# Performance work log

Hardware: AMD Instinct MI355X
Metric: run time of the kernel (lower is better)

Reference implementation:

```python
import jax, jax.numpy as jnp
import numpy as np

B, OBS, T, H = 4096, 16, 32, 512  # batch, encoder length, decode seq_len, hidden_size


def _lstm_cell(x, h, c, Wi, Wh, b):
    # PyTorch gate order: i, f, g, o. b = b_ih + b_hh (mathematically identical).
    g = x @ Wi.T + h @ Wh.T + b
    i, f, gg, o = jnp.split(g, 4, axis=-1)
    c = jax.nn.sigmoid(f) * c + jax.nn.sigmoid(i) * jnp.tanh(gg)
    h = jax.nn.sigmoid(o) * jnp.tanh(c)
    return h, c


def _encode(xs, Wi, Wh, b):
    # xs: [B, T, 4]; returns final (h, c), zero initial state as in nn.LSTM.
    def step(carry, x):
        h, c = _lstm_cell(x, carry[0], carry[1], Wi, Wh, b)
        return (h, c), None
    z = jnp.zeros((xs.shape[0], H), xs.dtype)
    (h, c), _ = jax.lax.scan(step, (z, z), jnp.swapaxes(xs, 0, 1))
    return h, c


def setup_inputs() -> dict:
    key = jax.random.key(0)
    ks = jax.random.split(key, 22)
    s = 0.05
    p = lambda k, shape: (jax.random.normal(k, shape, jnp.float32) * s)
    return {
        "speed": jax.random.normal(ks[0], (B, OBS, 4), jnp.float32),
        "pos": jax.random.normal(ks[1], (B, OBS, 4), jnp.float32),
        "enc_s_Wi": p(ks[2], (4 * H, 4)), "enc_s_Wh": p(ks[3], (4 * H, H)), "enc_s_b": p(ks[4], (4 * H,)),
        "enc_p_Wi": p(ks[5], (4 * H, 4)), "enc_p_Wh": p(ks[6], (4 * H, H)), "enc_p_b": p(ks[7], (4 * H,)),
        "dec_s_Wi": p(ks[8], (4 * H, 4)), "dec_s_Wh": p(ks[9], (4 * H, H)), "dec_s_b": p(ks[10], (4 * H,)),
        "dec_i_Wi": p(ks[11], (4 * H, 4)), "dec_i_Wh": p(ks[12], (4 * H, H)), "dec_i_b": p(ks[13], (4 * H,)),
        "W_fs": p(ks[14], (4, H)), "b_fs": p(ks[15], (4,)),
        "W_fc": p(ks[16], (2, H)), "b_fc": p(ks[17], (2,)),
        "W_emb": p(ks[18], (4, 2)), "b_emb": p(ks[19], (4,)),
    }


def reference(speed, pos,
              enc_s_Wi, enc_s_Wh, enc_s_b,
              enc_p_Wi, enc_p_Wh, enc_p_b,
              dec_s_Wi, dec_s_Wh, dec_s_b,
              dec_i_Wi, dec_i_Wh, dec_i_b,
              W_fs, b_fs, W_fc, b_fc, W_emb, b_emb):
    h_se, c_se = _encode(speed, enc_s_Wi, enc_s_Wh, enc_s_b)
    h_pe, c_pe = _encode(pos, enc_p_Wi, enc_p_Wh, enc_p_b)
    h_s, c_s = h_se + h_pe, c_se + c_pe
    h_i, c_i = h_s, c_s
    last_speed = speed[:, -1, :]
    last_pos = pos[:, -1, :]

    def step(carry, _):
        h_s, c_s, h_i, c_i, ls, lp = carry
        h_s, c_s = _lstm_cell(ls, h_s, c_s, dec_s_Wi, dec_s_Wh, dec_s_b)
        h_i, c_i = _lstm_cell(lp, h_i, c_i, dec_i_Wi, dec_i_Wh, dec_i_b)
        sp = jnp.clip(h_s @ W_fs.T + b_fs, -100.0, 100.0)        # Hardtanh(-100, 100)
        it = jax.nn.relu(h_i @ W_fc.T + b_fc)                     # fc_crossing
        ls = jax.lax.stop_gradient(sp)                            # .detach()
        lp = jax.lax.stop_gradient(jax.nn.relu(it @ W_emb.T + b_emb))  # pos_embedding(.).detach()
        return (h_s, c_s, h_i, c_i, ls, lp), (sp, jax.nn.softmax(it, axis=1))

    carry0 = (h_s, c_s, h_i, c_i, last_speed, last_pos)
    _, (speed_seq, cross_seq) = jax.lax.scan(step, carry0, None, length=T)
    speed_outputs = jnp.swapaxes(speed_seq, 0, 1)   # [B, T, 4]
    # Faithful to the source bug: intention_outputs is never accumulated, so the
    # returned crossing_outputs holds ONLY the last step's softmax: [B, 1, 2].
    crossing_outputs = cross_seq[-1][:, None, :]
    return speed_outputs, crossing_outputs
```

## Files before the change

kernel.cpp:

```cpp
#include <hip/hip_runtime.h>
#include <stdint.h>

#define H 512
#define KAUG 528
#define KT_N 33
#define LROW 536
#define NROW 32
#define WMAT_ELEMS (16 * KT_N * 4 * 512)
#define T_DEC 32
#define B_TOT 4096

typedef __attribute__((ext_vector_type(8))) short short8;
typedef __attribute__((ext_vector_type(16))) float floatx16;

__device__ __forceinline__ unsigned short f2bf(float x) {
  union { float f; unsigned int u; } v; v.f = x;
  unsigned int u = v.u;
  return (unsigned short)((u + 0x7FFFu + ((u >> 16) & 1u)) >> 16);
}
__device__ __forceinline__ float bf2f(unsigned short s) {
  union { unsigned int u; float f; } v; v.u = ((unsigned int)s) << 16;
  return v.f;
}
__device__ __forceinline__ float rcpf(float x) { return __builtin_amdgcn_rcpf(x); }
__device__ __forceinline__ float sigm(float x) { return rcpf(1.0f + __expf(-x)); }
__device__ __forceinline__ float tanh_f(float x) {
  return 1.0f - 2.0f * rcpf(1.0f + __expf(2.0f * x));
}

__global__ void prep_weights(
    const float* __restrict__ Wh_s, const float* __restrict__ Wi_s, const float* __restrict__ b_s,
    const float* __restrict__ Wh_p, const float* __restrict__ Wi_p, const float* __restrict__ b_p,
    const float* __restrict__ Wh_d, const float* __restrict__ Wi_d, const float* __restrict__ b_d,
    const float* __restrict__ Wh_i, const float* __restrict__ Wi_i, const float* __restrict__ b_i,
    short* __restrict__ wpack)
{
  int idx = blockIdx.x * 256 + threadIdx.x;
  const int per = 2048 * KAUG;
  if (idx >= 4 * per) return;
  int mat = idx / per;
  int rem = idx - mat * per;
  int n = rem / KAUG;
  int ka = rem - n * KAUG;
  const float* Wh; const float* Wi; const float* bb;
  if (mat == 0)      { Wh = Wh_s; Wi = Wi_s; bb = b_s; }
  else if (mat == 1) { Wh = Wh_p; Wi = Wi_p; bb = b_p; }
  else if (mat == 2) { Wh = Wh_d; Wi = Wi_d; bb = b_d; }
  else               { Wh = Wh_i; Wi = Wi_i; bb = b_i; }
  float v;
  if (ka < 512)      v = Wh[n * 512 + ka];
  else if (ka < 516) v = Wi[n * 4 + (ka - 512)];
  else if (ka == 516) v = bb[n];
  else               v = 0.0f;
  int g = n >> 9, ntL = (n >> 5) & 15, ni = n & 31;
  int kt = ka >> 4, kh = (ka >> 3) & 1, ks = ka & 7;
  int lanep = kh * 32 + ni;
  wpack[(size_t)mat * WMAT_ELEMS +
        (((((size_t)ntL * KT_N + kt) * 4 + g) << 9) + (lanep << 3) + ks)] = (short)f2bf(v);
}

__device__ __forceinline__ void lstm_step_mfma(
    const short* hl, const short* __restrict__ wm,
    int lane, int wv, float c_reg[16], float hnew[16])
{
  int arow = lane & 31, ahalf = lane >> 5;
  const short* aptr = hl + arow * LROW + ahalf * 8;
  const short* bp = wm + (size_t)wv * (KT_N * 4 * 512) + (lane << 3);
  floatx16 ai = (floatx16)0.0f, af = (floatx16)0.0f, ag = (floatx16)0.0f, ao = (floatx16)0.0f;
  #pragma unroll 3
  for (int kt = 0; kt < KT_N; ++kt) {
    short8 a  = *(const short8*)(aptr + kt * 16);
    short8 b0 = *(const short8*)(bp);
    short8 b1 = *(const short8*)(bp + 512);
    short8 b2 = *(const short8*)(bp + 1024);
    short8 b3 = *(const short8*)(bp + 1536);
    bp += 2048;
    ai = __builtin_amdgcn_mfma_f32_32x32x16_bf16(a, b0, ai, 0, 0, 0);
    af = __builtin_amdgcn_mfma_f32_32x32x16_bf16(a, b1, af, 0, 0, 0);
    ag = __builtin_amdgcn_mfma_f32_32x32x16_bf16(a, b2, ag, 0, 0, 0);
    ao = __builtin_amdgcn_mfma_f32_32x32x16_bf16(a, b3, ao, 0, 0, 0);
  }
  #pragma unroll
  for (int r = 0; r < 16; ++r) {
    float si = sigm(ai[r]);
    float sf = sigm(af[r]);
    float tg = tanh_f(ag[r]);
    float so = sigm(ao[r]);
    float cn = sf * c_reg[r] + si * tg;
    c_reg[r] = cn;
    hnew[r] = so * tanh_f(cn);
  }
}

__device__ __forceinline__ void write_h(short* hl, int lane, int wv, const float hnew[16]) {
  int arow = lane & 31, ahalf = lane >> 5;
  int col = (wv << 5) + arow;
  #pragma unroll
  for (int r = 0; r < 16; ++r) {
    int row = (r & 3) + ((r >> 2) << 3) + (ahalf << 2);
    hl[row * LROW + col] = (short)f2bf(hnew[r]);
  }
}

__global__ __launch_bounds__(1024) void lstm_encoder(
    const float* __restrict__ speed, const float* __restrict__ pos,
    const short* __restrict__ wpack,
    short* __restrict__ h_enc, float* __restrict__ c_enc)
{
  __shared__ short hl[NROW * LROW];
  int tid = threadIdx.x;
  int b = blockIdx.x;
  int xcd = b & 7, slot = b >> 3;
  int enc = xcd >> 2;
  int rg = slot * 4 + (xcd & 3);
  int r0 = rg * 32;
  const float* xin = enc ? pos : speed;
  const short* wm = wpack + (size_t)enc * WMAT_ELEMS;

  for (int i = tid; i < NROW * LROW; i += 1024) hl[i] = 0;
  __syncthreads();
  if (tid < 32) hl[tid * LROW + 516] = (short)0x3F80;
  if (tid < 128) {
    int r = tid >> 2, c = tid & 3;
    hl[r * LROW + 512 + c] = (short)f2bf(xin[(r0 + r) * 64 + c]);
  }
  __syncthreads();

  int lane = tid & 63, wv = tid >> 6;
  float c_reg[16];
  #pragma unroll
  for (int r = 0; r < 16; ++r) c_reg[r] = 0.0f;
  float hnew[16];

  for (int t = 0; t < 16; ++t) {
    lstm_step_mfma(hl, wm, lane, wv, c_reg, hnew);
    __syncthreads();
    write_h(hl, lane, wv, hnew);
    if (t < 15 && tid < 128) {
      int r = tid >> 2, c = tid & 3;
      hl[r * LROW + 512 + c] = (short)f2bf(xin[(r0 + r) * 64 + (t + 1) * 4 + c]);
    }
    __syncthreads();
  }

  for (int i = tid; i < 32 * 512; i += 1024) {
    int r = i >> 9, k = i & 511;
    h_enc[((size_t)(enc * B_TOT + r0 + r) << 9) + k] = hl[r * LROW + k];
  }
  int arow = lane & 31, ahalf = lane >> 5;
  int col = (wv << 5) + arow;
  #pragma unroll
  for (int r = 0; r < 16; ++r) {
    int row = (r & 3) + ((r >> 2) << 3) + (ahalf << 2);
    c_enc[((size_t)(enc * B_TOT + r0 + row) << 9) + col] = c_reg[r];
  }
}

__global__ __launch_bounds__(1024) void lstm_decoder(
    const float* __restrict__ speed, const float* __restrict__ pos,
    const short* __restrict__ wpack,
    const short* __restrict__ h_enc, const float* __restrict__ c_enc,
    const float* __restrict__ W_fs, const float* __restrict__ b_fs,
    const float* __restrict__ W_fc, const float* __restrict__ b_fc,
    const float* __restrict__ W_emb, const float* __restrict__ b_emb,
    float* __restrict__ out)
{
  __shared__ short hl[NROW * LROW];
  int tid = threadIdx.x;
  int b = blockIdx.x;
  int xcd = b & 7, slot = b >> 3;
  int chain = xcd >> 2;
  int rg = slot * 4 + (xcd & 3);
  int r0 = rg * 32;
  const short* wm = wpack + (size_t)(2 + chain) * WMAT_ELEMS;

  for (int i = tid; i < NROW * LROW; i += 1024) hl[i] = 0;
  __syncthreads();
  for (int i = tid; i < 32 * 512; i += 1024) {
    int r = i >> 9, k = i & 511;
    float h0 = bf2f((unsigned short)h_enc[((size_t)(r0 + r) << 9) + k])
             + bf2f((unsigned short)h_enc[((size_t)(B_TOT + r0 + r) << 9) + k]);
    hl[r * LROW + k] = (short)f2bf(h0);
  }
  if (tid < 32) hl[tid * LROW + 516] = (short)0x3F80;
  {
    const float* last = chain ? pos : speed;
    if (tid < 128) {
      int r = tid >> 2, c = tid & 3;
      hl[r * LROW + 512 + c] = (short)f2bf(last[(r0 + r) * 64 + 60 + c]);
    }
  }
  int lane = tid & 63, wv = tid >> 6;
  int arow = lane & 31, ahalf = lane >> 5;
  float c_reg[16];
  {
    int col = (wv << 5) + arow;
    #pragma unroll
    for (int r = 0; r < 16; ++r) {
      int row = (r & 3) + ((r >> 2) << 3) + (ahalf << 2);
      size_t gi = ((size_t)(r0 + row) << 9) + col;
      c_reg[r] = c_enc[gi] + c_enc[gi + (((size_t)B_TOT) << 9)];
    }
  }
  __syncthreads();

  float hnew[16];
  for (int t = 0; t < T_DEC; ++t) {
    lstm_step_mfma(hl, wm, lane, wv, c_reg, hnew);
    __syncthreads();
    write_h(hl, lane, wv, hnew);
    __syncthreads();
    for (int r = 0; r < 2; ++r) {
      int row = wv * 2 + r;
      const short8 hvs = *(const short8*)(hl + row * LROW + lane * 8);
      float hv[8];
      #pragma unroll
      for (int j = 0; j < 8; ++j) hv[j] = bf2f((unsigned short)hvs[j]);
      if (chain == 0) {
        float p0 = 0.f, p1 = 0.f, p2 = 0.f, p3 = 0.f;
        #pragma unroll
        for (int j = 0; j < 8; ++j) {
          p0 += hv[j] * W_fs[0 * 512 + lane * 8 + j];
          p1 += hv[j] * W_fs[1 * 512 + lane * 8 + j];
          p2 += hv[j] * W_fs[2 * 512 + lane * 8 + j];
          p3 += hv[j] * W_fs[3 * 512 + lane * 8 + j];
        }
        #pragma unroll
        for (int off = 32; off > 0; off >>= 1) {
          p0 += __shfl_xor(p0, off);
          p1 += __shfl_xor(p1, off);
          p2 += __shfl_xor(p2, off);
          p3 += __shfl_xor(p3, off);
        }
        float s0 = fminf(fmaxf(p0 + b_fs[0], -100.0f), 100.0f);
        float s1 = fminf(fmaxf(p1 + b_fs[1], -100.0f), 100.0f);
        float s2 = fminf(fmaxf(p2 + b_fs[2], -100.0f), 100.0f);
        float s3 = fminf(fmaxf(p3 + b_fs[3], -100.0f), 100.0f);
        if (lane < 4) {
          float v = (lane == 0) ? s0 : (lane == 1) ? s1 : (lane == 2) ? s2 : s3;
          out[(size_t)(r0 + row) * 128 + t * 4 + lane] = v;
          hl[row * LROW + 512 + lane] = (short)f2bf(v);
        }
      } else {
        float p0 = 0.f, p1 = 0.f;
        #pragma unroll
        for (int j = 0; j < 8; ++j) {
          p0 += hv[j] * W_fc[0 * 512 + lane * 8 + j];
          p1 += hv[j] * W_fc[1 * 512 + lane * 8 + j];
        }
        #pragma unroll
        for (int off = 32; off > 0; off >>= 1) {
          p0 += __shfl_xor(p0, off);
          p1 += __shfl_xor(p1, off);
        }
        float it0 = fmaxf(p0 + b_fc[0], 0.0f);
        float it1 = fmaxf(p1 + b_fc[1], 0.0f);
        if (lane < 4) {
          float lp = fmaxf(W_emb[lane * 2] * it0 + W_emb[lane * 2 + 1] * it1 + b_emb[lane], 0.0f);
          hl[row * LROW + 512 + lane] = (short)f2bf(lp);
        }
        if (t == T_DEC - 1 && lane < 2) {
          float m = fmaxf(it0, it1);
          float e0 = __expf(it0 - m), e1 = __expf(it1 - m);
          float v = ((lane == 0) ? e0 : e1) * rcpf(e0 + e1);
          out[(size_t)524288 + (size_t)(r0 + row) * 2 + lane] = v;
        }
      }
    }
    __syncthreads();
  }
}

extern "C" void kernel_launch(void* const* d_in, const int* in_sizes, int n_in,
                              void* d_out, int out_size, void* d_ws, size_t ws_size,
                              hipStream_t stream)
{
  const float* speed    = (const float*)d_in[0];
  const float* pos      = (const float*)d_in[1];
  const float* enc_s_Wi = (const float*)d_in[2];
  const float* enc_s_Wh = (const float*)d_in[3];
  const float* enc_s_b  = (const float*)d_in[4];
  const float* enc_p_Wi = (const float*)d_in[5];
  const float* enc_p_Wh = (const float*)d_in[6];
  const float* enc_p_b  = (const float*)d_in[7];
  const float* dec_s_Wi = (const float*)d_in[8];
  const float* dec_s_Wh = (const float*)d_in[9];
  const float* dec_s_b  = (const float*)d_in[10];
  const float* dec_i_Wi = (const float*)d_in[11];
  const float* dec_i_Wh = (const float*)d_in[12];
  const float* dec_i_b  = (const float*)d_in[13];
  const float* W_fs     = (const float*)d_in[14];
  const float* b_fs     = (const float*)d_in[15];
  const float* W_fc     = (const float*)d_in[16];
  const float* b_fc     = (const float*)d_in[17];
  const float* W_emb    = (const float*)d_in[18];
  const float* b_emb    = (const float*)d_in[19];
  float* out = (float*)d_out;

  char* ws = (char*)d_ws;
  short* wpack = (short*)ws;
  short* h_enc = (short*)(ws + 8650752);
  float* c_enc = (float*)(ws + 17039360);

  prep_weights<<<16896, 256, 0, stream>>>(
      enc_s_Wh, enc_s_Wi, enc_s_b,
      enc_p_Wh, enc_p_Wi, enc_p_b,
      dec_s_Wh, dec_s_Wi, dec_s_b,
      dec_i_Wh, dec_i_Wi, dec_i_b,
      wpack);
  lstm_encoder<<<256, 1024, 0, stream>>>(speed, pos, wpack, h_enc, c_enc);
  lstm_decoder<<<256, 1024, 0, stream>>>(speed, pos, wpack, h_enc, c_enc,
                                         W_fs, b_fs, W_fc, b_fc, W_emb, b_emb, out);
}
```

Before: 1.249 ms.

## Store decoder LSTM weights in scaled FP8 and dequantize to bf16 in-register

Decoder recurrent weights are packed as e4m3 FP8, pre-scaled by 64, in a new prep kernel with a matching layout. The decoder step loads half the bytes per k-tile and converts them back to bf16 with cvt_pk_f32_fp8 and perm before the bf16 MFMAs, then undoes the scale on the gate pre-activations. The goal is to halve the weight bandwidth the decoder streams from L2/HBM at every timestep. In exchange it adds per-element conversion ALU work and loses precision in the decoder weights, which may hurt accuracy.

```diff
diff --git a/kernel.cpp b/kernel.cpp
--- a/kernel.cpp
+++ b/kernel.cpp
@@ -7,11 +7,17 @@
 #define LROW 536
 #define NROW 32
 #define WMAT_ELEMS (16 * KT_N * 4 * 512)
+#define WMAT8_BYTES 1081344
+#define NTL8_BYTES 67584
 #define T_DEC 32
 #define B_TOT 4096
+#define SCL 0.015625f
 
 typedef __attribute__((ext_vector_type(8))) short short8;
 typedef __attribute__((ext_vector_type(16))) float floatx16;
+typedef __attribute__((ext_vector_type(2))) float float2v;
+typedef __attribute__((ext_vector_type(4))) unsigned int uint4v;
+typedef __attribute__((ext_vector_type(2))) unsigned int uint2v;
 
 __device__ __forceinline__ unsigned short f2bf(float x) {
   union { float f; unsigned int u; } v; v.f = x;
@@ -28,25 +34,59 @@
   return 1.0f - 2.0f * rcpf(1.0f + __expf(2.0f * x));
 }
 
+__device__ __forceinline__ unsigned char f2e4m3(float f) {
+  unsigned int u = __float_as_uint(f);
+  unsigned int s = (u >> 24) & 0x80u;
+  float a = fabsf(f);
+  if (!(a < 464.0f)) return (unsigned char)(s | 0x7Eu);
+  if (a < 0.0009765625f) return (unsigned char)s;
+  int e = (int)((__float_as_uint(a) >> 23) & 0xFF) - 127;
+  int q = (e < -6 ? -6 : e) - 3;
+  float sc  = __uint_as_float((unsigned int)((127 - q) << 23));
+  float isc = __uint_as_float((unsigned int)((127 + q) << 23));
+  float n = rintf(a * sc);
+  float r = n * isc;
+  if (r == 0.0f) return (unsigned char)s;
+  int e2 = (int)((__float_as_uint(r) >> 23) & 0xFF) - 127;
+  unsigned int bits;
+  if (e2 < -6) {
+    bits = (unsigned int)(r * 512.0f + 0.5f);
+  } else {
+    float msc = __uint_as_float((unsigned int)((127 - (e2 - 3)) << 23));
+    unsigned int mant = (unsigned int)(r * msc + 0.5f);
+    bits = ((unsigned int)(e2 + 7) << 3) | (mant & 7u);
+  }
+  return (unsigned char)(s | bits);
+}
+
+__device__ __forceinline__ short8 dq8(unsigned int d0, unsigned int d1) {
+  float2v p0 = __builtin_amdgcn_cvt_pk_f32_fp8(d0, false);
+  float2v p1 = __builtin_amdgcn_cvt_pk_f32_fp8(d0, true);
+  float2v p2 = __builtin_amdgcn_cvt_pk_f32_fp8(d1, false);
+  float2v p3 = __builtin_amdgcn_cvt_pk_f32_fp8(d1, true);
+  union { unsigned int u[4]; short8 s; } r;
+  r.u[0] = __builtin_amdgcn_perm(__float_as_uint(p0[1]), __float_as_uint(p0[0]), 0x07060302u);
+  r.u[1] = __builtin_amdgcn_perm(__float_as_uint(p1[1]), __float_as_uint(p1[0]), 0x07060302u);
+  r.u[2] = __builtin_amdgcn_perm(__float_as_uint(p2[1]), __float_as_uint(p2[0]), 0x07060302u);
+  r.u[3] = __builtin_amdgcn_perm(__float_as_uint(p3[1]), __float_as_uint(p3[0]), 0x07060302u);
+  return r.s;
+}
+
 __global__ void prep_weights(
     const float* __restrict__ Wh_s, const float* __restrict__ Wi_s, const float* __restrict__ b_s,
     const float* __restrict__ Wh_p, const float* __restrict__ Wi_p, const float* __restrict__ b_p,
-    const float* __restrict__ Wh_d, const float* __restrict__ Wi_d, const float* __restrict__ b_d,
-    const float* __restrict__ Wh_i, const float* __restrict__ Wi_i, const float* __restrict__ b_i,
     short* __restrict__ wpack)
 {
   int idx = blockIdx.x * 256 + threadIdx.x;
   const int per = 2048 * KAUG;
-  if (idx >= 4 * per) return;
+  if (idx >= 2 * per) return;
   int mat = idx / per;
   int rem = idx - mat * per;
   int n = rem / KAUG;
   int ka = rem - n * KAUG;
-  const float* Wh; const float* Wi; const float* bb;
-  if (mat == 0)      { Wh = Wh_s; Wi = Wi_s; bb = b_s; }
-  else if (mat == 1) { Wh = Wh_p; Wi = Wi_p; bb = b_p; }
-  else if (mat == 2) { Wh = Wh_d; Wi = Wi_d; bb = b_d; }
-  else               { Wh = Wh_i; Wi = Wi_i; bb = b_i; }
+  const float* Wh = mat ? Wh_p : Wh_s;
+  const float* Wi = mat ? Wi_p : Wi_s;
+  const float* bb = mat ? b_p  : b_s;
   float v;
   if (ka < 512)      v = Wh[n * 512 + ka];
   else if (ka < 516) v = Wi[n * 4 + (ka - 512)];
@@ -57,6 +97,45 @@
   int lanep = kh * 32 + ni;
   wpack[(size_t)mat * WMAT_ELEMS +
         (((((size_t)ntL * KT_N + kt) * 4 + g) << 9) + (lanep << 3) + ks)] = (short)f2bf(v);
+}
+
+__global__ void prep_fp8(
+    const float* __restrict__ Wh_d, const float* __restrict__ Wi_d, const float* __restrict__ b_d,
+    const float* __restrict__ Wh_i, const float* __restrict__ Wi_i, const float* __restrict__ b_i,
+    unsigned char* __restrict__ wpack8)
+{
+  int idx = blockIdx.x * 256 + threadIdx.x;
+  if (idx >= 2 * WMAT8_BYTES) return;
+  int mat = idx / WMAT8_BYTES;
+  int rem = idx - mat * WMAT8_BYTES;
+  int ntL = rem / NTL8_BYTES;
+  int off = rem - ntL * NTL8_BYTES;
+  int g, lane, kt, ks;
+  if (off < 65536) {
+    int p = off >> 12;
+    g = (off >> 10) & 3;
+    lane = (off >> 4) & 63;
+    int j = off & 15;
+    kt = 2 * p + (j >> 3);
+    ks = j & 7;
+  } else {
+    int t = off - 65536;
+    g = t >> 9;
+    lane = (t >> 3) & 63;
+    ks = t & 7;
+    kt = 32;
+  }
+  int n = g * 512 + ntL * 32 + (lane & 31);
+  int ka = kt * 16 + (lane >> 5) * 8 + ks;
+  const float* Wh = mat ? Wh_i : Wh_d;
+  const float* Wi = mat ? Wi_i : Wi_d;
+  const float* bb = mat ? b_i  : b_d;
+  float v;
+  if (ka < 512)       v = Wh[n * 512 + ka];
+  else if (ka < 516)  v = Wi[n * 4 + (ka - 512)];
+  else if (ka == 516) v = bb[n];
+  else                v = 0.0f;
+  wpack8[idx] = f2e4m3(v * 64.0f);
 }
 
 __device__ __forceinline__ void lstm_step_mfma(
@@ -92,6 +171,54 @@
   }
 }
 
+__device__ __forceinline__ void lstm_step_mfma_fp8(
+    const short* hl, const unsigned char* __restrict__ wmb,
+    int lane, int wv, float c_reg[16], float hnew[16])
+{
+  int arow = lane & 31, ahalf = lane >> 5;
+  const short* aptr = hl + arow * LROW + ahalf * 8;
+  const unsigned char* base = wmb + (size_t)wv * NTL8_BYTES;
+  const uint4v* bp = (const uint4v*)(base + (lane << 4));
+  floatx16 ai = (floatx16)0.0f, af = (floatx16)0.0f, ag = (floatx16)0.0f, ao = (floatx16)0.0f;
+  #pragma unroll 1
+  for (int p = 0; p < 16; ++p) {
+    uint4v di = bp[0];
+    uint4v df = bp[64];
+    uint4v dg = bp[128];
+    uint4v dd = bp[192];
+    short8 a0 = *(const short8*)(aptr + p * 32);
+    short8 a1 = *(const short8*)(aptr + p * 32 + 16);
+    bp += 256;
+    ai = __builtin_amdgcn_mfma_f32_32x32x16_bf16(a0, dq8(di[0], di[1]), ai, 0, 0, 0);
+    af = __builtin_amdgcn_mfma_f32_32x32x16_bf16(a0, dq8(df[0], df[1]), af, 0, 0, 0);
+    ag = __builtin_amdgcn_mfma_f32_32x32x16_bf16(a0, dq8(dg[0], dg[1]), ag, 0, 0, 0);
+    ao = __builtin_amdgcn_mfma_f32_32x32x16_bf16(a0, dq8(dd[0], dd[1]), ao, 0, 0, 0);
+    ai = __builtin_amdgcn_mfma_f32_32x32x16_bf16(a1, dq8(di[2], di[3]), ai, 0, 0, 0);
+    af = __builtin_amdgcn_mfma_f32_32x32x16_bf16(a1, dq8(df[2], df[3]), af, 0, 0, 0);
+    ag = __builtin_amdgcn_mfma_f32_32x32x16_bf16(a1, dq8(dg[2], dg[3]), ag, 0, 0, 0);
+    ao = __builtin_amdgcn_mfma_f32_32x32x16_bf16(a1, dq8(dd[2], dd[3]), ao, 0, 0, 0);
+  }
+  {
+    const uint2v* tp = (const uint2v*)(base + 65536 + (lane << 3));
+    uint2v ti = tp[0], tf = tp[64], tg = tp[128], td = tp[192];
+    short8 a0 = *(const short8*)(aptr + 512);
+    ai = __builtin_amdgcn_mfma_f32_32x32x16_bf16(a0, dq8(ti[0], ti[1]), ai, 0, 0, 0);
+    af = __builtin_amdgcn_mfma_f32_32x32x16_bf16(a0, dq8(tf[0], tf[1]), af, 0, 0, 0);
+    ag = __builtin_amdgcn_mfma_f32_32x32x16_bf16(a0, dq8(tg[0], tg[1]), ag, 0, 0, 0);
+    ao = __builtin_amdgcn_mfma_f32_32x32x16_bf16(a0, dq8(td[0], td[1]), ao, 0, 0, 0);
+  }
+  #pragma unroll
+  for (int r = 0; r < 16; ++r) {
+    float si = sigm(ai[r] * SCL);
+    float sf = sigm(af[r] * SCL);
+    float tg = tanh_f(ag[r] * SCL);
+    float so = sigm(ao[r] * SCL);
+    float cn = sf * c_reg[r] + si * tg;
+    c_reg[r] = cn;
+    hnew[r] = so * tanh_f(cn);
+  }
+}
+
 __device__ __forceinline__ void write_h(short* hl, int lane, int wv, const float hnew[16]) {
   int arow = lane & 31, ahalf = lane >> 5;
   int col = (wv << 5) + arow;
@@ -158,7 +285,7 @@
 
 __global__ __launch_bounds__(1024) void lstm_decoder(
     const float* __restrict__ speed, const float* __restrict__ pos,
-    const short* __restrict__ wpack,
+    const unsigned char* __restrict__ wpack8,
     const short* __restrict__ h_enc, const float* __restrict__ c_enc,
     const float* __restrict__ W_fs, const float* __restrict__ b_fs,
     const float* __restrict__ W_fc, const float* __restrict__ b_fc,
@@ -172,7 +299,7 @@
   int chain = xcd >> 2;
   int rg = slot * 4 + (xcd & 3);
   int r0 = rg * 32;
-  const short* wm = wpack + (size_t)(2 + chain) * WMAT_ELEMS;
+  const unsigned char* wm8 = wpack8 + (size_t)chain * WMAT8_BYTES;
 
   for (int i = tid; i < NROW * LROW; i += 1024) hl[i] = 0;
   __syncthreads();
@@ -206,7 +333,7 @@
 
   float hnew[16];
   for (int t = 0; t < T_DEC; ++t) {
-    lstm_step_mfma(hl, wm, lane, wv, c_reg, hnew);
+    lstm_step_mfma_fp8(hl, wm8, lane, wv, c_reg, hnew);
     __syncthreads();
     write_h(hl, lane, wv, hnew);
     __syncthreads();
@@ -298,17 +425,20 @@
   float* out = (float*)d_out;
 
   char* ws = (char*)d_ws;
-  short* wpack = (short*)ws;
-  short* h_enc = (short*)(ws + 8650752);
-  float* c_enc = (float*)(ws + 17039360);
-
-  prep_weights<<<16896, 256, 0, stream>>>(
+  short* wpack          = (short*)ws;
+  unsigned char* wpack8 = (unsigned char*)(ws + 4325376);
+  short* h_enc          = (short*)(ws + 6488064);
+  float* c_enc          = (float*)(ws + 14876672);
+
+  prep_weights<<<8448, 256, 0, stream>>>(
       enc_s_Wh, enc_s_Wi, enc_s_b,
       enc_p_Wh, enc_p_Wi, enc_p_b,
+      wpack);
+  prep_fp8<<<8448, 256, 0, stream>>>(
       dec_s_Wh, dec_s_Wi, dec_s_b,
       dec_i_Wh, dec_i_Wi, dec_i_b,
-      wpack);
+      wpack8);
   lstm_encoder<<<256, 1024, 0, stream>>>(speed, pos, wpack, h_enc, c_enc);
-  lstm_decoder<<<256, 1024, 0, stream>>>(speed, pos, wpack, h_enc, c_enc,
+  lstm_decoder<<<256, 1024, 0, stream>>>(speed, pos, wpack8, h_enc, c_enc,
                                          W_fs, b_fs, W_fc, b_fc, W_emb, b_emb, out);
 }
```

Result: slower. 1.377 ms (+10.3%).

## Double-buffer hidden state in LDS and software-pipeline weight loads in MFMA loop

Applied to the files above, without the earlier changes.

The hidden-state LDS tile becomes two ping-pong buffers, so each LSTM step reads one buffer and writes the other. This removes one __syncthreads per timestep in both the encoder and decoder. The MFMA K-loop is restructured to prefetch the next two k-tiles of weight fragments into registers ahead of use, overlapping global loads with matrix ops. The cost is double the LDS footprint and more live registers for the prefetched B fragments, which could affect occupancy or cause spills.

```diff
diff --git a/kernel.cpp b/kernel.cpp
--- a/kernel.cpp
+++ b/kernel.cpp
@@ -27,6 +27,8 @@
 __device__ __forceinline__ float tanh_f(float x) {
   return 1.0f - 2.0f * rcpf(1.0f + __expf(2.0f * x));
 }
+
+#define MFMA(A, B, C) __builtin_amdgcn_mfma_f32_32x32x16_bf16(A, B, C, 0, 0, 0)
 
 __global__ void prep_weights(
     const float* __restrict__ Wh_s, const float* __restrict__ Wi_s, const float* __restrict__ b_s,
@@ -67,18 +69,33 @@
   const short* aptr = hl + arow * LROW + ahalf * 8;
   const short* bp = wm + (size_t)wv * (KT_N * 4 * 512) + (lane << 3);
   floatx16 ai = (floatx16)0.0f, af = (floatx16)0.0f, ag = (floatx16)0.0f, ao = (floatx16)0.0f;
-  #pragma unroll 3
-  for (int kt = 0; kt < KT_N; ++kt) {
-    short8 a  = *(const short8*)(aptr + kt * 16);
-    short8 b0 = *(const short8*)(bp);
-    short8 b1 = *(const short8*)(bp + 512);
-    short8 b2 = *(const short8*)(bp + 1024);
-    short8 b3 = *(const short8*)(bp + 1536);
-    bp += 2048;
-    ai = __builtin_amdgcn_mfma_f32_32x32x16_bf16(a, b0, ai, 0, 0, 0);
-    af = __builtin_amdgcn_mfma_f32_32x32x16_bf16(a, b1, af, 0, 0, 0);
-    ag = __builtin_amdgcn_mfma_f32_32x32x16_bf16(a, b2, ag, 0, 0, 0);
-    ao = __builtin_amdgcn_mfma_f32_32x32x16_bf16(a, b3, ao, 0, 0, 0);
+  short8 b00 = *(const short8*)(bp +    0), b01 = *(const short8*)(bp +  512);
+  short8 b02 = *(const short8*)(bp + 1024), b03 = *(const short8*)(bp + 1536);
+  short8 b10 = *(const short8*)(bp + 2048), b11 = *(const short8*)(bp + 2560);
+  short8 b12 = *(const short8*)(bp + 3072), b13 = *(const short8*)(bp + 3584);
+  #pragma unroll 2
+  for (int kt = 0; kt < 32; kt += 2) {
+    short8 a0 = *(const short8*)(aptr + kt * 16);
+    ai = MFMA(a0, b00, ai); af = MFMA(a0, b01, af);
+    ag = MFMA(a0, b02, ag); ao = MFMA(a0, b03, ao);
+    {
+      const short* np = bp + (kt + 2) * 2048;
+      b00 = *(const short8*)(np);        b01 = *(const short8*)(np + 512);
+      b02 = *(const short8*)(np + 1024); b03 = *(const short8*)(np + 1536);
+    }
+    short8 a1 = *(const short8*)(aptr + kt * 16 + 16);
+    ai = MFMA(a1, b10, ai); af = MFMA(a1, b11, af);
+    ag = MFMA(a1, b12, ag); ao = MFMA(a1, b13, ao);
+    if (kt < 30) {
+      const short* np = bp + (kt + 3) * 2048;
+      b10 = *(const short8*)(np);        b11 = *(const short8*)(np + 512);
+      b12 = *(const short8*)(np + 1024); b13 = *(const short8*)(np + 1536);
+    }
+  }
+  {
+    short8 a0 = *(const short8*)(aptr + 512);
+    ai = MFMA(a0, b00, ai); af = MFMA(a0, b01, af);
+    ag = MFMA(a0, b02, ag); ao = MFMA(a0, b03, ao);
   }
   #pragma unroll
   for (int r = 0; r < 16; ++r) {
@@ -107,7 +124,7 @@
     const short* __restrict__ wpack,
     short* __restrict__ h_enc, float* __restrict__ c_enc)
 {
-  __shared__ short hl[NROW * LROW];
+  __shared__ short hl[2][NROW * LROW];
   int tid = threadIdx.x;
   int b = blockIdx.x;
   int xcd = b & 7, slot = b >> 3;
@@ -117,12 +134,15 @@
   const float* xin = enc ? pos : speed;
   const short* wm = wpack + (size_t)enc * WMAT_ELEMS;
 
-  for (int i = tid; i < NROW * LROW; i += 1024) hl[i] = 0;
+  {
+    short* hz = &hl[0][0];
+    for (int i = tid; i < 2 * NROW * LROW; i += 1024) hz[i] = 0;
+  }
   __syncthreads();
-  if (tid < 32) hl[tid * LROW + 516] = (short)0x3F80;
+  if (tid < 64) hl[tid >> 5][(tid & 31) * LROW + 516] = (short)0x3F80;
   if (tid < 128) {
     int r = tid >> 2, c = tid & 3;
-    hl[r * LROW + 512 + c] = (short)f2bf(xin[(r0 + r) * 64 + c]);
+    hl[0][r * LROW + 512 + c] = (short)f2bf(xin[(r0 + r) * 64 + c]);
   }
   __syncthreads();
 
@@ -133,19 +153,20 @@
   float hnew[16];
 
   for (int t = 0; t < 16; ++t) {
-    lstm_step_mfma(hl, wm, lane, wv, c_reg, hnew);
-    __syncthreads();
-    write_h(hl, lane, wv, hnew);
+    const short* cb = hl[t & 1];
+    short* nb = &hl[(t + 1) & 1][0];
+    lstm_step_mfma(cb, wm, lane, wv, c_reg, hnew);
+    write_h(nb, lane, wv, hnew);
     if (t < 15 && tid < 128) {
       int r = tid >> 2, c = tid & 3;
-      hl[r * LROW + 512 + c] = (short)f2bf(xin[(r0 + r) * 64 + (t + 1) * 4 + c]);
+      nb[r * LROW + 512 + c] = (short)f2bf(xin[(r0 + r) * 64 + (t + 1) * 4 + c]);
     }
     __syncthreads();
   }
 
   for (int i = tid; i < 32 * 512; i += 1024) {
     int r = i >> 9, k = i & 511;
-    h_enc[((size_t)(enc * B_TOT + r0 + r) << 9) + k] = hl[r * LROW + k];
+    h_enc[((size_t)(enc * B_TOT + r0 + r) << 9) + k] = hl[0][r * LROW + k];
   }
   int arow = lane & 31, ahalf = lane >> 5;
   int col = (wv << 5) + arow;
@@ -165,7 +186,7 @@
     const float* __restrict__ W_emb, const float* __restrict__ b_emb,
     float* __restrict__ out)
 {
-  __shared__ short hl[NROW * LROW];
+  __shared__ short hl[2][NROW * LROW];
   int tid = threadIdx.x;
   int b = blockIdx.x;
   int xcd = b & 7, slot = b >> 3;
@@ -174,20 +195,23 @@
   int r0 = rg * 32;
   const short* wm = wpack + (size_t)(2 + chain) * WMAT_ELEMS;
 
-  for (int i = tid; i < NROW * LROW; i += 1024) hl[i] = 0;
+  {
+    short* hz = &hl[0][0];
+    for (int i = tid; i < 2 * NROW * LROW; i += 1024) hz[i] = 0;
+  }
   __syncthreads();
   for (int i = tid; i < 32 * 512; i += 1024) {
     int r = i >> 9, k = i & 511;
     float h0 = bf2f((unsigned short)h_enc[((size_t)(r0 + r) << 9) + k])
              + bf2f((unsigned short)h_enc[((size_t)(B_TOT + r0 + r) << 9) + k]);
-    hl[r * LROW + k] = (short)f2bf(h0);
-  }
-  if (tid < 32) hl[tid * LROW + 516] = (short)0x3F80;
+    hl[0][r * LROW + k] = (short)f2bf(h0);
+  }
+  if (tid < 64) hl[tid >> 5][(tid & 31) * LROW + 516] = (short)0x3F80;
   {
     const float* last = chain ? pos : speed;
     if (tid < 128) {
       int r = tid >> 2, c = tid & 3;
-      hl[r * LROW + 512 + c] = (short)f2bf(last[(r0 + r) * 64 + 60 + c]);
+      hl[0][r * LROW + 512 + c] = (short)f2bf(last[(r0 + r) * 64 + 60 + c]);
     }
   }
   int lane = tid & 63, wv = tid >> 6;
@@ -206,13 +230,14 @@
 
   float hnew[16];
   for (int t = 0; t < T_DEC; ++t) {
-    lstm_step_mfma(hl, wm, lane, wv, c_reg, hnew);
-    __syncthreads();
-    write_h(hl, lane, wv, hnew);
+    const short* cb = hl[t & 1];
+    short* nb = &hl[(t + 1) & 1][0];
+    lstm_step_mfma(cb, wm, lane, wv, c_reg, hnew);
+    write_h(nb, lane, wv, hnew);
     __syncthreads();
     for (int r = 0; r < 2; ++r) {
       int row = wv * 2 + r;
-      const short8 hvs = *(const short8*)(hl + row * LROW + lane * 8);
+      const short8 hvs = *(const short8*)(nb + row * LROW + lane * 8);
       float hv[8];
       #pragma unroll
       for (int j = 0; j < 8; ++j) hv[j] = bf2f((unsigned short)hvs[j]);
@@ -239,7 +264,7 @@
         if (lane < 4) {
           float v = (lane == 0) ? s0 : (lane == 1) ? s1 : (lane == 2) ? s2 : s3;
           out[(size_t)(r0 + row) * 128 + t * 4 + lane] = v;
-          hl[row * LROW + 512 + lane] = (short)f2bf(v);
+          nb[row * LROW + 512 + lane] = (short)f2bf(v);
         }
       } else {
         float p0 = 0.f, p1 = 0.f;
@@ -257,7 +282,7 @@
         float it1 = fmaxf(p1 + b_fc[1], 0.0f);
         if (lane < 4) {
           float lp = fmaxf(W_emb[lane * 2] * it0 + W_emb[lane * 2 + 1] * it1 + b_emb[lane], 0.0f);
-          hl[row * LROW + 512 + lane] = (short)f2bf(lp);
+          nb[row * LROW + 512 + lane] = (short)f2bf(lp);
         }
         if (t == T_DEC - 1 && lane < 2) {
           float m = fmaxf(it0, it1);
```

Result: slower. 1.452 ms (+16.2%).

## Stream LSTM weights through per-wave LDS ring buffer with async global_load_lds

Applied to the files above, without the earlier changes.

Replaces direct global register loads of the packed gate weights with a three-slot per-wave LDS ring filled by global_load_lds, prefetching two half-tiles ahead and waiting with explicit vmcnt. It also restructures the per-step barriers: the last k-tile (the augmented input and bias column) is computed after a sync so the h write and next-input write can share one barrier, removing a __syncthreads per step. This aims to hide weight-fetch latency behind MFMAs. In exchange it adds about 96KB of LDS per block plus hand-managed wait counts, and it depends on subtle ordering of the reads and writes to hl across steps.

```diff
diff --git a/kernel.cpp b/kernel.cpp
--- a/kernel.cpp
+++ b/kernel.cpp
@@ -7,11 +7,16 @@
 #define LROW 536
 #define NROW 32
 #define WMAT_ELEMS (16 * KT_N * 4 * 512)
+#define NTL_ELEMS  (KT_N * 4 * 512)
+#define RING_W 3072
 #define T_DEC 32
 #define B_TOT 4096
 
 typedef __attribute__((ext_vector_type(8))) short short8;
 typedef __attribute__((ext_vector_type(16))) float floatx16;
+
+typedef __attribute__((address_space(1))) const void* gas_p;
+typedef __attribute__((address_space(3))) void* las_p;
 
 __device__ __forceinline__ unsigned short f2bf(float x) {
   union { float f; unsigned int u; } v; v.f = x;
@@ -26,6 +31,13 @@
 __device__ __forceinline__ float sigm(float x) { return rcpf(1.0f + __expf(-x)); }
 __device__ __forceinline__ float tanh_f(float x) {
   return 1.0f - 2.0f * rcpf(1.0f + __expf(2.0f * x));
+}
+
+#define MFMA(A, B, C) __builtin_amdgcn_mfma_f32_32x32x16_bf16(A, B, C, 0, 0, 0)
+
+__device__ __forceinline__ void stage_half(const short* src, short* dst) {
+  __builtin_amdgcn_global_load_lds((gas_p)(src),       (las_p)(dst),       16, 0, 0);
+  __builtin_amdgcn_global_load_lds((gas_p)(src + 512), (las_p)(dst + 512), 16, 0, 0);
 }
 
 __global__ void prep_weights(
@@ -59,40 +71,47 @@
         (((((size_t)ntL * KT_N + kt) * 4 + g) << 9) + (lanep << 3) + ks)] = (short)f2bf(v);
 }
 
-__device__ __forceinline__ void lstm_step_mfma(
-    const short* hl, const short* __restrict__ wm,
-    int lane, int wv, float c_reg[16], float hnew[16])
-{
-  int arow = lane & 31, ahalf = lane >> 5;
-  const short* aptr = hl + arow * LROW + ahalf * 8;
-  const short* bp = wm + (size_t)wv * (KT_N * 4 * 512) + (lane << 3);
-  floatx16 ai = (floatx16)0.0f, af = (floatx16)0.0f, ag = (floatx16)0.0f, ao = (floatx16)0.0f;
-  #pragma unroll 3
-  for (int kt = 0; kt < KT_N; ++kt) {
+__device__ __forceinline__ void lstm_gates_staged(
+    const short* aptr, const short* wmn_lane, short* slots, int lane, int& p,
+    floatx16& ai, floatx16& af, floatx16& ag, floatx16& ao)
+{
+  #pragma unroll 1
+  for (int kt = 0; kt < 32; ++kt) {
+    int ps = p + 2; if (ps >= 3) ps -= 3;
+    stage_half(wmn_lane + (2 * kt + 2) * 1024, slots + ps * 1024);
+    asm volatile("s_waitcnt vmcnt(4)" ::: "memory");
     short8 a  = *(const short8*)(aptr + kt * 16);
-    short8 b0 = *(const short8*)(bp);
-    short8 b1 = *(const short8*)(bp + 512);
-    short8 b2 = *(const short8*)(bp + 1024);
-    short8 b3 = *(const short8*)(bp + 1536);
-    bp += 2048;
-    ai = __builtin_amdgcn_mfma_f32_32x32x16_bf16(a, b0, ai, 0, 0, 0);
-    af = __builtin_amdgcn_mfma_f32_32x32x16_bf16(a, b1, af, 0, 0, 0);
-    ag = __builtin_amdgcn_mfma_f32_32x32x16_bf16(a, b2, ag, 0, 0, 0);
-    ao = __builtin_amdgcn_mfma_f32_32x32x16_bf16(a, b3, ao, 0, 0, 0);
-  }
-  #pragma unroll
-  for (int r = 0; r < 16; ++r) {
-    float si = sigm(ai[r]);
-    float sf = sigm(af[r]);
-    float tg = tanh_f(ag[r]);
-    float so = sigm(ao[r]);
-    float cn = sf * c_reg[r] + si * tg;
-    c_reg[r] = cn;
-    hnew[r] = so * tanh_f(cn);
-  }
-}
-
-__device__ __forceinline__ void write_h(short* hl, int lane, int wv, const float hnew[16]) {
+    short8 b0 = *(const short8*)(slots + p * 1024 + (lane << 3));
+    short8 b1 = *(const short8*)(slots + p * 1024 + 512 + (lane << 3));
+    ai = MFMA(a, b0, ai); af = MFMA(a, b1, af);
+    stage_half(wmn_lane + (2 * kt + 3) * 1024, slots + p * 1024);
+    asm volatile("s_waitcnt vmcnt(4)" ::: "memory");
+    int p1 = p + 1; if (p1 >= 3) p1 -= 3;
+    short8 b2 = *(const short8*)(slots + p1 * 1024 + (lane << 3));
+    short8 b3 = *(const short8*)(slots + p1 * 1024 + 512 + (lane << 3));
+    ag = MFMA(a, b2, ag); ao = MFMA(a, b3, ao);
+    p = ps;
+  }
+  __syncthreads();
+  {
+    int ps = p + 2; if (ps >= 3) ps -= 3;
+    stage_half(wmn_lane, slots + ps * 1024);
+    asm volatile("s_waitcnt vmcnt(4)" ::: "memory");
+    short8 a  = *(const short8*)(aptr + 512);
+    short8 b0 = *(const short8*)(slots + p * 1024 + (lane << 3));
+    short8 b1 = *(const short8*)(slots + p * 1024 + 512 + (lane << 3));
+    ai = MFMA(a, b0, ai); af = MFMA(a, b1, af);
+    stage_half(wmn_lane + 1024, slots + p * 1024);
+    asm volatile("s_waitcnt vmcnt(4)" ::: "memory");
+    int p1 = p + 1; if (p1 >= 3) p1 -= 3;
+    short8 b2 = *(const short8*)(slots + p1 * 1024 + (lane << 3));
+    short8 b3 = *(const short8*)(slots + p1 * 1024 + 512 + (lane << 3));
+    ag = MFMA(a, b2, ag); ao = MFMA(a, b3, ao);
+    p = ps;
+  }
+}
+
+__device__ __forceinline__ void write_h16(short* hl, int lane, int wv, const float hnew[16]) {
   int arow = lane & 31, ahalf = lane >> 5;
   int col = (wv << 5) + arow;
   #pragma unroll
@@ -108,6 +127,7 @@
     short* __restrict__ h_enc, float* __restrict__ c_enc)
 {
   __shared__ short hl[NROW * LROW];
+  __shared__ short ring[16 * RING_W];
   int tid = threadIdx.x;
   int b = blockIdx.x;
   int xcd = b & 7, slot = b >> 3;
@@ -116,6 +136,14 @@
   int r0 = rg * 32;
   const float* xin = enc ? pos : speed;
   const short* wm = wpack + (size_t)enc * WMAT_ELEMS;
+  int lane = tid & 63, wv = tid >> 6;
+  int arow = lane & 31, ahalf = lane >> 5;
+
+  const short* wmn_lane = wm + (size_t)wv * NTL_ELEMS + (lane << 3);
+  short* slots = ring + wv * RING_W;
+  stage_half(wmn_lane, slots);
+  stage_half(wmn_lane + 1024, slots + 1024);
+  int p = 0;
 
   for (int i = tid; i < NROW * LROW; i += 1024) hl[i] = 0;
   __syncthreads();
@@ -126,28 +154,38 @@
   }
   __syncthreads();
 
-  int lane = tid & 63, wv = tid >> 6;
   float c_reg[16];
   #pragma unroll
   for (int r = 0; r < 16; ++r) c_reg[r] = 0.0f;
   float hnew[16];
+  const short* aptr = hl + arow * LROW + ahalf * 8;
 
   for (int t = 0; t < 16; ++t) {
-    lstm_step_mfma(hl, wm, lane, wv, c_reg, hnew);
+    floatx16 ai = (floatx16)0.0f, af = (floatx16)0.0f,
+             ag = (floatx16)0.0f, ao = (floatx16)0.0f;
+    lstm_gates_staged(aptr, wmn_lane, slots, lane, p, ai, af, ag, ao);
+    #pragma unroll
+    for (int r = 0; r < 16; ++r) {
+      float si = sigm(ai[r]);
+      float sf = sigm(af[r]);
+      float tg = tanh_f(ag[r]);
+      float so = sigm(ao[r]);
+      float cn = sf * c_reg[r] + si * tg;
+      c_reg[r] = cn;
+      hnew[r] = so * tanh_f(cn);
+    }
+    write_h16(hl, lane, wv, hnew);
     __syncthreads();
-    write_h(hl, lane, wv, hnew);
     if (t < 15 && tid < 128) {
       int r = tid >> 2, c = tid & 3;
       hl[r * LROW + 512 + c] = (short)f2bf(xin[(r0 + r) * 64 + (t + 1) * 4 + c]);
     }
-    __syncthreads();
   }
 
   for (int i = tid; i < 32 * 512; i += 1024) {
     int r = i >> 9, k = i & 511;
     h_enc[((size_t)(enc * B_TOT + r0 + r) << 9) + k] = hl[r * LROW + k];
   }
-  int arow = lane & 31, ahalf = lane >> 5;
   int col = (wv << 5) + arow;
   #pragma unroll
   for (int r = 0; r < 16; ++r) {
@@ -166,6 +204,7 @@
     float* __restrict__ out)
 {
   __shared__ short hl[NROW * LROW];
+  __shared__ short ring[16 * RING_W];
   int tid = threadIdx.x;
   int b = blockIdx.x;
   int xcd = b & 7, slot = b >> 3;
@@ -173,6 +212,14 @@
   int rg = slot * 4 + (xcd & 3);
   int r0 = rg * 32;
   const short* wm = wpack + (size_t)(2 + chain) * WMAT_ELEMS;
+  int lane = tid & 63, wv = tid >> 6;
+  int arow = lane & 31, ahalf = lane >> 5;
+
+  const short* wmn_lane = wm + (size_t)wv * NTL_ELEMS + (lane << 3);
+  short* slots = ring + wv * RING_W;
+  stage_half(wmn_lane, slots);
+  stage_half(wmn_lane + 1024, slots + 1024);
+  int p = 0;
 
   for (int i = tid; i < NROW * LROW; i += 1024) hl[i] = 0;
   __syncthreads();
@@ -190,8 +237,7 @@
       hl[r * LROW + 512 + c] = (short)f2bf(last[(r0 + r) * 64 + 60 + c]);
     }
   }
-  int lane = tid & 63, wv = tid >> 6;
-  int arow = lane & 31, ahalf = lane >> 5;
+
   float c_reg[16];
   {
     int col = (wv << 5) + arow;
@@ -204,12 +250,27 @@
   }
   __syncthreads();
 
+  const short* aptr = hl + arow * LROW + ahalf * 8;
   float hnew[16];
   for (int t = 0; t < T_DEC; ++t) {
-    lstm_step_mfma(hl, wm, lane, wv, c_reg, hnew);
+    floatx16 ai = (floatx16)0.0f, af = (floatx16)0.0f,
+             ag = (floatx16)0.0f, ao = (floatx16)0.0f;
+    lstm_gates_staged(aptr, wmn_lane, slots, lane, p, ai, af, ag, ao);
+
+    #pragma unroll
+    for (int r = 0; r < 16; ++r) {
+      float si = sigm(ai[r]);
+      float sf = sigm(af[r]);
+      float tg = tanh_f(ag[r]);
+      float so = sigm(ao[r]);
+      float cn = sf * c_reg[r] + si * tg;
+      c_reg[r] = cn;
+      hnew[r] = so * tanh_f(cn);
+    }
+    write_h16(hl, lane, wv, hnew);
     __syncthreads();
-    write_h(hl, lane, wv, hnew);
-    __syncthreads();
+
+    #pragma unroll 1
     for (int r = 0; r < 2; ++r) {
       int row = wv * 2 + r;
       const short8 hvs = *(const short8*)(hl + row * LROW + lane * 8);
@@ -267,7 +328,6 @@
         }
       }
     }
-    __syncthreads();
   }
 }
 
```

Result: slower. 1.439 ms (+15.2%).
